# Optimization experiments

Measured on AMD Instinct MI355X. Metric: run time of the kernel, lower is better.

The kernel has to match this reference:

```python
import jax, jax.numpy as jnp
import numpy as np

N = 10000   # nodes (Hi-C bins)
E = 640000  # directed edges
H = 2       # attention heads
C = 512     # per-head out channels
NEG_SLOPE = 0.2

def _leaky_relu(v):
    return jnp.where(v >= 0, v, NEG_SLOPE * v)

def setup_inputs() -> dict:
    key = jax.random.key(0)
    ks = jax.random.split(key, 16)
    s = 0.02
    return {
        "x": jax.random.normal(ks[0], (N, 512), jnp.float32),
        "edge_index": jax.random.randint(ks[1], (2, E), 0, N, dtype=jnp.int64),
        "W": jax.random.normal(ks[2], (512, H * C), jnp.float32) * s,
        "att_src": jax.random.normal(ks[3], (H, C), jnp.float32) * s,
        "att_dst": jax.random.normal(ks[4], (H, C), jnp.float32) * s,
        "bias_conv": jnp.zeros((H * C,), jnp.float32),
        "Wa": jax.random.normal(ks[5], (1024, 256), jnp.float32) * s,
        "ba": jnp.zeros((256,), jnp.float32),
        "W1": jax.random.normal(ks[6], (256, 128), jnp.float32) * s,
        "b1": jnp.zeros((128,), jnp.float32),
        "W2": jax.random.normal(ks[7], (128, 64), jnp.float32) * s,
        "b2": jnp.zeros((64,), jnp.float32),
        "W3": jax.random.normal(ks[8], (64, 3), jnp.float32) * s,
        "b3": jnp.zeros((3,), jnp.float32),
    }

def reference(x, edge_index, W, att_src, att_dst, bias_conv,
              Wa, ba, W1, b1, W2, b2, W3, b3):
    n = x.shape[0]
    # PyG GATConv default: add self loops
    loop = jnp.arange(n, dtype=edge_index.dtype)
    src = jnp.concatenate([edge_index[0], loop])  # [E+N]
    dst = jnp.concatenate([edge_index[1], loop])
    # linear projection -> [N, H, C]
    h = (x @ W).reshape(n, H, C)
    a_src = jnp.einsum('nhc,hc->nh', h, att_src)  # [N, H]
    a_dst = jnp.einsum('nhc,hc->nh', h, att_dst)
    e = _leaky_relu(a_src[src] + a_dst[dst])      # [E+N, H]
    # segment softmax over destination nodes
    m = jax.ops.segment_max(e, dst, num_segments=n)
    ex = jnp.exp(e - m[dst])
    denom = jax.ops.segment_sum(ex, dst, num_segments=n)
    alpha = ex / denom[dst]                        # [E+N, H]
    # weighted scatter-add aggregation
    out = jax.ops.segment_sum(h[src] * alpha[..., None], dst, num_segments=n)
    out = out.reshape(n, H * C) + bias_conv        # concat heads -> [N, 1024]
    # MLP (dropout is identity in eval)
    y = jax.nn.relu(out)
    y = jax.nn.relu(y @ Wa + ba)
    y = jax.nn.relu(y @ W1 + b1)
    y = jax.nn.relu(y @ W2 + b2)
    y = y @ W3 + b3                                # [N, 3]
    # cdist p=2 via gram trick, grad-safe sqrt at 0
    sq = jnp.sum(y * y, axis=1)
    d2 = jnp.maximum(sq[:, None] + sq[None, :] - 2.0 * (y @ y.T), 0.0)
    pos = d2 > 0
    return jnp.where(pos, jnp.sqrt(jnp.where(pos, d2, 1.0)), 0.0)  # [N, N]
```

## Files before the change

kernel.cpp:

```cpp
#include <hip/hip_runtime.h>
#include <hip/hip_bf16.h>
#include <math.h>

#define N_NODES 10000
#define NE      640000
#define NTOT    (NE + N_NODES)
#define HC      1024
#define CC      512
#define SLOT    256

typedef __attribute__((ext_vector_type(8))) short bf16x8;
typedef __attribute__((ext_vector_type(4))) float f32x4;

__device__ __forceinline__ float lrelu(float v) { return v >= 0.f ? v : 0.2f * v; }

__device__ __forceinline__ void split1(float f, ushort& h, ushort& l) {
    unsigned u = __float_as_uint(f);
    unsigned hb = (u + 0x7FFFu + ((u >> 16) & 1u)) >> 16;
    float fh = __uint_as_float(hb << 16);
    float fl = f - fh;
    unsigned ul = __float_as_uint(fl);
    unsigned lb = (ul + 0x7FFFu + ((ul >> 16) & 1u)) >> 16;
    h = (ushort)hb; l = (ushort)lb;
}

__global__ __launch_bounds__(256) void transp_split(
    const float* __restrict__ Win, int K, int N,
    ushort* __restrict__ Th, ushort* __restrict__ Tl,
    float* __restrict__ zbuf, int zn)
{
    __shared__ float tile[32][33];
    int n0 = blockIdx.x * 32, k0 = blockIdx.y * 32;
    int tx = threadIdx.x & 31, ty = threadIdx.x >> 5;
    int gtid = (blockIdx.y * gridDim.x + blockIdx.x) * 256 + threadIdx.x;
    if (gtid < zn) zbuf[gtid] = 0.f;
    #pragma unroll
    for (int r = 0; r < 4; ++r)
        tile[ty + r * 8][tx] = Win[(size_t)(k0 + ty + r * 8) * N + n0 + tx];
    __syncthreads();
    #pragma unroll
    for (int r = 0; r < 4; ++r) {
        int n = ty + r * 8;
        float f = tile[tx][n];
        ushort h, l;
        split1(f, h, l);
        Th[(size_t)(n0 + n) * K + k0 + tx] = h;
        Tl[(size_t)(n0 + n) * K + k0 + tx] = l;
    }
}

template<int RELU_BIAS, int ATT, int SPLITA>
__global__ __launch_bounds__(256) void gemm_bf16x3(
    const ushort* __restrict__ Ah, const ushort* __restrict__ Al,
    const float* __restrict__ Af,
    const ushort* __restrict__ Bh, const ushort* __restrict__ Bl,
    const float* __restrict__ biasC,
    const float* __restrict__ attS, const float* __restrict__ attD,
    float* __restrict__ aS, float* __restrict__ aD,
    float* __restrict__ C, int M, int N, int K)
{
    __shared__ __align__(16) ushort sAh[4][128][8];
    __shared__ __align__(16) ushort sAl[4][128][8];
    __shared__ __align__(16) ushort sBh[4][128][8];
    __shared__ __align__(16) ushort sBl[4][128][8];
    const int bm = blockIdx.y * 128;
    const int bn = blockIdx.x * 128;
    const int tid = threadIdx.x;
    const int lane = tid & 63;
    const int w = tid >> 6;
    const int wm = (w >> 1) * 64, wn = (w & 1) * 64;
    const int l15 = lane & 15, l4 = lane >> 4;

    f32x4 acc[4][4];
    #pragma unroll
    for (int i = 0; i < 4; ++i)
        #pragma unroll
        for (int j = 0; j < 4; ++j)
            acc[i][j] = (f32x4){0.f, 0.f, 0.f, 0.f};

    for (int k0 = 0; k0 < K; k0 += 32) {
        #pragma unroll
        for (int qi = 0; qi < 4; ++qi) {
            int Q = qi * 256 + tid;
            int m = Q >> 3;
            int kq = (Q & 7) * 4;
            int gr = bm + m;
            ushort4 vh = make_ushort4(0, 0, 0, 0), vl = vh;
            if (SPLITA) {
                if (gr < M) {
                    float4 av = *(const float4*)(Af + (size_t)gr * K + k0 + kq);
                    split1(av.x, vh.x, vl.x);
                    split1(av.y, vh.y, vl.y);
                    split1(av.z, vh.z, vl.z);
                    split1(av.w, vh.w, vl.w);
                }
            } else if (gr < M) {
                vh = *(const ushort4*)(Ah + (size_t)gr * K + k0 + kq);
                vl = *(const ushort4*)(Al + (size_t)gr * K + k0 + kq);
            }
            *(ushort4*)&sAh[kq >> 3][m][kq & 7] = vh;
            *(ushort4*)&sAl[kq >> 3][m][kq & 7] = vl;
            ushort4 wh = *(const ushort4*)(Bh + (size_t)(bn + m) * K + k0 + kq);
            ushort4 wl = *(const ushort4*)(Bl + (size_t)(bn + m) * K + k0 + kq);
            *(ushort4*)&sBh[kq >> 3][m][kq & 7] = wh;
            *(ushort4*)&sBl[kq >> 3][m][kq & 7] = wl;
        }
        __syncthreads();
        bf16x8 ah[4], al[4], bh[4], bl[4];
        #pragma unroll
        for (int i = 0; i < 4; ++i) {
            ah[i] = *(const bf16x8*)&sAh[l4][wm + i * 16 + l15][0];
            al[i] = *(const bf16x8*)&sAl[l4][wm + i * 16 + l15][0];
            bh[i] = *(const bf16x8*)&sBh[l4][wn + i * 16 + l15][0];
            bl[i] = *(const bf16x8*)&sBl[l4][wn + i * 16 + l15][0];
        }
        #pragma unroll
        for (int i = 0; i < 4; ++i)
            #pragma unroll
            for (int j = 0; j < 4; ++j) {
                acc[i][j] = __builtin_amdgcn_mfma_f32_16x16x32_bf16(ah[i], bh[j], acc[i][j], 0, 0, 0);
                acc[i][j] = __builtin_amdgcn_mfma_f32_16x16x32_bf16(ah[i], bl[j], acc[i][j], 0, 0, 0);
                acc[i][j] = __builtin_amdgcn_mfma_f32_16x16x32_bf16(al[i], bh[j], acc[i][j], 0, 0, 0);
            }
        __syncthreads();
    }
    const int head = ATT ? ((bn + wn) >> 9) : 0;
    #pragma unroll
    for (int i = 0; i < 4; ++i) {
        #pragma unroll
        for (int r = 0; r < 4; ++r) {
            int row = bm + wm + i * 16 + l4 * 4 + r;
            if (row >= M) continue;
            float ps = 0.f, pd = 0.f;
            #pragma unroll
            for (int j = 0; j < 4; ++j) {
                int col = bn + wn + j * 16 + l15;
                float v = acc[i][j][r];
                if (RELU_BIAS) v = fmaxf(v + biasC[col], 0.f);
                C[(size_t)row * N + col] = v;
                if (ATT) {
                    int cc = col & (CC - 1);
                    ps += v * attS[head * CC + cc];
                    pd += v * attD[head * CC + cc];
                }
            }
            if (ATT) {
                #pragma unroll
                for (int o = 1; o < 16; o <<= 1) {
                    ps += __shfl_xor(ps, o);
                    pd += __shfl_xor(pd, o);
                }
                if (l15 == 0) {
                    atomicAdd(&aS[row * 2 + head], ps);
                    atomicAdd(&aD[row * 2 + head], pd);
                }
            }
        }
    }
}

template<int RELU_OUT, int MLP3>
__global__ __launch_bounds__(256) void gemm64(
    const float* __restrict__ A, const float* __restrict__ B,
    const float* __restrict__ biasC, float* __restrict__ C,
    const float* __restrict__ W3, const float* __restrict__ b3,
    float* __restrict__ y, float* __restrict__ sq,
    int M, int N, int K)
{
    __shared__ float As[16][68];
    __shared__ float Bs[16][68];
    const int bm = blockIdx.y * 64;
    const int bn = blockIdx.x * 64;
    const int tid = threadIdx.x;
    const int tx = tid & 15, ty = tid >> 4;

    const int arow  = tid >> 2;
    const int acol4 = (tid & 3) * 4;
    const int brow  = tid >> 4;
    const int bcol4 = (tid & 15) * 4;

    float acc[4][4] = {};

    for (int k0 = 0; k0 < K; k0 += 16) {
        int gr = bm + arow;
        float4 av = make_float4(0.f, 0.f, 0.f, 0.f);
        if (gr < M) av = *(const float4*)(A + (size_t)gr * K + k0 + acol4);
        As[acol4 + 0][arow] = av.x;
        As[acol4 + 1][arow] = av.y;
        As[acol4 + 2][arow] = av.z;
        As[acol4 + 3][arow] = av.w;
        float4 bv = *(const float4*)(B + (size_t)(k0 + brow) * N + bn + bcol4);
        *(float4*)&Bs[brow][bcol4] = bv;
        __syncthreads();
        #pragma unroll
        for (int k = 0; k < 16; ++k) {
            float a0 = As[k][ty * 4 + 0], a1 = As[k][ty * 4 + 1];
            float a2 = As[k][ty * 4 + 2], a3 = As[k][ty * 4 + 3];
            float b0 = Bs[k][tx * 4 + 0], b1 = Bs[k][tx * 4 + 1];
            float b2 = Bs[k][tx * 4 + 2], b3 = Bs[k][tx * 4 + 3];
            acc[0][0] += a0 * b0; acc[0][1] += a0 * b1; acc[0][2] += a0 * b2; acc[0][3] += a0 * b3;
            acc[1][0] += a1 * b0; acc[1][1] += a1 * b1; acc[1][2] += a1 * b2; acc[1][3] += a1 * b3;
            acc[2][0] += a2 * b0; acc[2][1] += a2 * b1; acc[2][2] += a2 * b2; acc[2][3] += a2 * b3;
            acc[3][0] += a3 * b0; acc[3][1] += a3 * b1; acc[3][2] += a3 * b2; acc[3][3] += a3 * b3;
        }
        __syncthreads();
    }
    #pragma unroll
    for (int i = 0; i < 4; ++i) {
        int row = bm + ty * 4 + i;
        if (row >= M) continue;
        if (MLP3) {
            float p0 = 0.f, p1 = 0.f, p2 = 0.f;
            #pragma unroll
            for (int j = 0; j < 4; ++j) {
                int col = tx * 4 + j;
                float v = fmaxf(acc[i][j] + biasC[col], 0.f);
                p0 += v * W3[col * 3 + 0];
                p1 += v * W3[col * 3 + 1];
                p2 += v * W3[col * 3 + 2];
            }
            #pragma unroll
            for (int o = 1; o < 16; o <<= 1) {
                p0 += __shfl_xor(p0, o);
                p1 += __shfl_xor(p1, o);
                p2 += __shfl_xor(p2, o);
            }
            if (tx == 0) {
                p0 += b3[0]; p1 += b3[1]; p2 += b3[2];
                y[row * 3 + 0] = p0; y[row * 3 + 1] = p1; y[row * 3 + 2] = p2;
                sq[row] = p0 * p0 + p1 * p1 + p2 * p2;
            }
        } else {
            #pragma unroll
            for (int j = 0; j < 4; ++j) {
                int col = bn + tx * 4 + j;
                float v = acc[i][j] + biasC[col];
                if (RELU_OUT) v = fmaxf(v, 0.f);
                C[(size_t)row * N + col] = v;
            }
        }
    }
}

__global__ __launch_bounds__(256) void scatter_stats(
    const int* __restrict__ ei,
    const float2* __restrict__ a_src2, const float2* __restrict__ a_dst2,
    int* __restrict__ cnt, float* __restrict__ denom,
    int2* __restrict__ pack0, int2* __restrict__ pack1)
{
    int e = blockIdx.x * blockDim.x + threadIdx.x;
    if (e >= NTOT) return;
    int s, d;
    if (e < NE) { s = ei[e]; d = ei[NE + e]; } else { s = d = e - NE; }
    float2 as = a_src2[s];
    float2 ad = a_dst2[d];
    float e0 = expf(lrelu(as.x + ad.x));
    float e1 = expf(lrelu(as.y + ad.y));
    int pos = atomicAdd(&cnt[d], 1);
    int slot = (d << 8) + pos;
    pack0[slot] = make_int2(s, __float_as_int(e0));
    pack1[slot] = make_int2(s, __float_as_int(e1));
    atomicAdd(&denom[d * 2 + 0], e0);
    atomicAdd(&denom[d * 2 + 1], e1);
}

__global__ __launch_bounds__(256) void aggregate_w4(
    const int* __restrict__ cnt,
    const int2* __restrict__ pack0, const int2* __restrict__ pack1,
    const float* __restrict__ denom, const float* __restrict__ bias_conv,
    const float* __restrict__ h,
    ushort* __restrict__ outh, ushort* __restrict__ outl)
{
    int wave = threadIdx.x >> 6;
    int lane = threadIdx.x & 63;
    int g    = lane >> 4;
    int l16  = lane & 15;
    int d = blockIdx.x * 4 + wave;
    int chunk = blockIdx.y;
    int cb = chunk * 64;
    int hd = chunk >> 3;
    const int2* __restrict__ pk = ((hd == 0) ? pack0 : pack1) + (d << 8);
    int cd = cnt[d];
    float inv = 1.f / denom[d * 2 + hd];
    const float* hbase = h + cb + l16 * 4;
    float4 ac0 = make_float4(0.f, 0.f, 0.f, 0.f);
    float4 ac1 = make_float4(0.f, 0.f, 0.f, 0.f);
    float4 ac2 = make_float4(0.f, 0.f, 0.f, 0.f);
    float4 ac3 = make_float4(0.f, 0.f, 0.f, 0.f);
    int i = g;
    for (; i + 12 < cd; i += 16) {
        int2 e0 = pk[i];
        int2 e1 = pk[i + 4];
        int2 e2 = pk[i + 8];
        int2 e3 = pk[i + 12];
        const float4 h0 = *(const float4*)(hbase + (size_t)e0.x * HC);
        const float4 h1 = *(const float4*)(hbase + (size_t)e1.x * HC);
        const float4 h2 = *(const float4*)(hbase + (size_t)e2.x * HC);
        const float4 h3 = *(const float4*)(hbase + (size_t)e3.x * HC);
        float a0 = __int_as_float(e0.y), a1 = __int_as_float(e1.y);
        float a2 = __int_as_float(e2.y), a3 = __int_as_float(e3.y);
        ac0.x += a0 * h0.x; ac0.y += a0 * h0.y; ac0.z += a0 * h0.z; ac0.w += a0 * h0.w;
        ac1.x += a1 * h1.x; ac1.y += a1 * h1.y; ac1.z += a1 * h1.z; ac1.w += a1 * h1.w;
        ac2.x += a2 * h2.x; ac2.y += a2 * h2.y; ac2.z += a2 * h2.z; ac2.w += a2 * h2.w;
        ac3.x += a3 * h3.x; ac3.y += a3 * h3.y; ac3.z += a3 * h3.z; ac3.w += a3 * h3.w;
    }
    for (; i < cd; i += 4) {
        int2 e0 = pk[i];
        float a0 = __int_as_float(e0.y);
        const float4 h0 = *(const float4*)(hbase + (size_t)e0.x * HC);
        ac0.x += a0 * h0.x; ac0.y += a0 * h0.y; ac0.z += a0 * h0.z; ac0.w += a0 * h0.w;
    }
    ac0.x += ac1.x + ac2.x + ac3.x;
    ac0.y += ac1.y + ac2.y + ac3.y;
    ac0.z += ac1.z + ac2.z + ac3.z;
    ac0.w += ac1.w + ac2.w + ac3.w;
    ac0.x += __shfl_xor(ac0.x, 16); ac0.y += __shfl_xor(ac0.y, 16);
    ac0.z += __shfl_xor(ac0.z, 16); ac0.w += __shfl_xor(ac0.w, 16);
    ac0.x += __shfl_xor(ac0.x, 32); ac0.y += __shfl_xor(ac0.y, 32);
    ac0.z += __shfl_xor(ac0.z, 32); ac0.w += __shfl_xor(ac0.w, 32);
    if (g == 0) {
        int c0 = cb + l16 * 4;
        float v[4];
        v[0] = fmaxf(ac0.x * inv + bias_conv[c0 + 0], 0.f);
        v[1] = fmaxf(ac0.y * inv + bias_conv[c0 + 1], 0.f);
        v[2] = fmaxf(ac0.z * inv + bias_conv[c0 + 2], 0.f);
        v[3] = fmaxf(ac0.w * inv + bias_conv[c0 + 3], 0.f);
        ushort hh[4], ll[4];
        #pragma unroll
        for (int j = 0; j < 4; ++j) split1(v[j], hh[j], ll[j]);
        *(ushort4*)(outh + (size_t)d * HC + c0) = make_ushort4(hh[0], hh[1], hh[2], hh[3]);
        *(ushort4*)(outl + (size_t)d * HC + c0) = make_ushort4(ll[0], ll[1], ll[2], ll[3]);
    }
}

__global__ __launch_bounds__(256) void pdist(
    const float* __restrict__ y, const float* __restrict__ sq,
    float* __restrict__ out)
{
    int i = blockIdx.y;
    int j0 = (blockIdx.x * 256 + threadIdx.x) * 4;
    if (j0 >= N_NODES) return;
    float yi0 = y[i * 3 + 0], yi1 = y[i * 3 + 1], yi2 = y[i * 3 + 2];
    float si = sq[i];
    float res[4];
    #pragma unroll
    for (int t = 0; t < 4; ++t) {
        int j = j0 + t;
        float d2 = si + sq[j] - 2.f * (yi0 * y[j * 3 + 0] + yi1 * y[j * 3 + 1] + yi2 * y[j * 3 + 2]);
        d2 = fmaxf(d2, 0.f);
        res[t] = d2 > 0.f ? sqrtf(d2) : 0.f;
    }
    *(float4*)(out + (size_t)i * N_NODES + j0) = make_float4(res[0], res[1], res[2], res[3]);
}

extern "C" void kernel_launch(void* const* d_in, const int* in_sizes, int n_in,
                              void* d_out, int out_size, void* d_ws, size_t ws_size,
                              hipStream_t stream) {
    const float* x         = (const float*)d_in[0];
    const int*   ei        = (const int*)d_in[1];
    const float* W         = (const float*)d_in[2];
    const float* att_src   = (const float*)d_in[3];
    const float* att_dst   = (const float*)d_in[4];
    const float* bias_conv = (const float*)d_in[5];
    const float* Wa        = (const float*)d_in[6];
    const float* ba        = (const float*)d_in[7];
    const float* W1        = (const float*)d_in[8];
    const float* b1        = (const float*)d_in[9];
    const float* W2        = (const float*)d_in[10];
    const float* b2        = (const float*)d_in[11];
    const float* W3        = (const float*)d_in[12];
    const float* b3        = (const float*)d_in[13];
    float* out = (float*)d_out;

    float*  h        = out;
    ushort* outh     = (ushort*)(out + 10240000);
    ushort* outl     = (ushort*)(out + 15360000);
    float*  y1       = out + 20480000;
    float*  y2       = out + 23040000;
    float*  a_src    = out + 24960000;
    float*  a_dst    = out + 24980000;
    int*    cnt      = (int*)(out + 25000000);
    float*  denom    = out + 25010240;
    int2*   pack0    = (int2*)(out + 25500000);
    int2*   pack1    = (int2*)(out + 30700000);
    ushort* Wth      = (ushort*)(out + 36000000);
    ushort* Wtl      = (ushort*)(out + 36300000);
    ushort* Wath     = (ushort*)(out + 36600000);
    ushort* Watl     = (ushort*)(out + 36800000);

    float* y  = (float*)d_ws;
    float* sq = (float*)d_ws + 30000;

    transp_split<<<dim3(1024 / 32, 512 / 32), 256, 0, stream>>>(
        W, 512, 1024, Wth, Wtl, a_src, 40000);
    transp_split<<<dim3(256 / 32, 1024 / 32), 256, 0, stream>>>(
        Wa, 1024, 256, Wath, Watl, (float*)cnt, 30240);

    gemm_bf16x3<0, 1, 1><<<dim3(1024 / 128, (N_NODES + 127) / 128), 256, 0, stream>>>(
        nullptr, nullptr, x, Wth, Wtl, nullptr, att_src, att_dst, a_src, a_dst,
        h, N_NODES, 1024, 512);

    scatter_stats<<<(NTOT + 255) / 256, 256, 0, stream>>>(
        ei, (const float2*)a_src, (const float2*)a_dst, cnt, denom, pack0, pack1);

    aggregate_w4<<<dim3(N_NODES / 4, 16), 256, 0, stream>>>(
        cnt, pack0, pack1, denom, bias_conv, h, outh, outl);

    gemm_bf16x3<1, 0, 0><<<dim3(256 / 128, (N_NODES + 127) / 128), 256, 0, stream>>>(
        outh, outl, nullptr, Wath, Watl, ba, nullptr, nullptr, nullptr, nullptr,
        y1, N_NODES, 256, 1024);
    gemm64<1, 0><<<dim3(128 / 64, (N_NODES + 63) / 64), 256, 0, stream>>>(
        y1, W1, b1, y2, nullptr, nullptr, nullptr, nullptr, N_NODES, 128, 256);
    gemm64<1, 1><<<dim3(1, (N_NODES + 63) / 64), 256, 0, stream>>>(
        y2, W2, b2, nullptr, W3, b3, y, sq, N_NODES, 64, 128);

    pdist<<<dim3((N_NODES + 1023) / 1024, N_NODES), 256, 0, stream>>>(y, sq, out);
}
```

Before: 551.8 us.

## Store h in per-chunk layout, fold softmax denom into aggregation, pack y with sq

The projection GEMM now writes h in a chunk-major layout ([16 chunks][N][64]), so each aggregation block gathers from a compact 2.5MB slice that fits in cache better. The softmax denominator is summed inside the aggregation loop instead of with float atomics in scatter_stats, which removes two atomics per edge and the denom buffer. y and its squared norm are packed into one float4 per node, so pdist does a single vector load per node instead of four scalar loads. The trade-off is that the alpha sum is recomputed by every chunk, 16 times per node.

```diff
diff --git a/kernel.cpp b/kernel.cpp
--- a/kernel.cpp
+++ b/kernel.cpp
@@ -8,6 +8,7 @@
 #define HC      1024
 #define CC      512
 #define SLOT    256
+#define CHN     (N_NODES * 64)
 
 typedef __attribute__((ext_vector_type(8))) short bf16x8;
 typedef __attribute__((ext_vector_type(4))) float f32x4;
@@ -137,11 +138,13 @@
                 int col = bn + wn + j * 16 + l15;
                 float v = acc[i][j][r];
                 if (RELU_BIAS) v = fmaxf(v + biasC[col], 0.f);
-                C[(size_t)row * N + col] = v;
                 if (ATT) {
+                    C[(size_t)(col >> 6) * CHN + (size_t)row * 64 + (col & 63)] = v;
                     int cc = col & (CC - 1);
                     ps += v * attS[head * CC + cc];
                     pd += v * attD[head * CC + cc];
+                } else {
+                    C[(size_t)row * N + col] = v;
                 }
             }
             if (ATT) {
@@ -164,7 +167,7 @@
     const float* __restrict__ A, const float* __restrict__ B,
     const float* __restrict__ biasC, float* __restrict__ C,
     const float* __restrict__ W3, const float* __restrict__ b3,
-    float* __restrict__ y, float* __restrict__ sq,
+    float4* __restrict__ y4,
     int M, int N, int K)
 {
     __shared__ float As[16][68];
@@ -227,8 +230,7 @@
             }
             if (tx == 0) {
                 p0 += b3[0]; p1 += b3[1]; p2 += b3[2];
-                y[row * 3 + 0] = p0; y[row * 3 + 1] = p1; y[row * 3 + 2] = p2;
-                sq[row] = p0 * p0 + p1 * p1 + p2 * p2;
+                y4[row] = make_float4(p0, p1, p2, p0 * p0 + p1 * p1 + p2 * p2);
             }
         } else {
             #pragma unroll
@@ -245,7 +247,7 @@
 __global__ __launch_bounds__(256) void scatter_stats(
     const int* __restrict__ ei,
     const float2* __restrict__ a_src2, const float2* __restrict__ a_dst2,
-    int* __restrict__ cnt, float* __restrict__ denom,
+    int* __restrict__ cnt,
     int2* __restrict__ pack0, int2* __restrict__ pack1)
 {
     int e = blockIdx.x * blockDim.x + threadIdx.x;
@@ -260,15 +262,13 @@
     int slot = (d << 8) + pos;
     pack0[slot] = make_int2(s, __float_as_int(e0));
     pack1[slot] = make_int2(s, __float_as_int(e1));
-    atomicAdd(&denom[d * 2 + 0], e0);
-    atomicAdd(&denom[d * 2 + 1], e1);
 }
 
 __global__ __launch_bounds__(256) void aggregate_w4(
     const int* __restrict__ cnt,
     const int2* __restrict__ pack0, const int2* __restrict__ pack1,
-    const float* __restrict__ denom, const float* __restrict__ bias_conv,
-    const float* __restrict__ h,
+    const float* __restrict__ bias_conv,
+    const float* __restrict__ hc,
     ushort* __restrict__ outh, ushort* __restrict__ outl)
 {
     int wave = threadIdx.x >> 6;
@@ -281,24 +281,25 @@
     int hd = chunk >> 3;
     const int2* __restrict__ pk = ((hd == 0) ? pack0 : pack1) + (d << 8);
     int cd = cnt[d];
-    float inv = 1.f / denom[d * 2 + hd];
-    const float* hbase = h + cb + l16 * 4;
+    const float* hbase = hc + (size_t)chunk * CHN + l16 * 4;
     float4 ac0 = make_float4(0.f, 0.f, 0.f, 0.f);
     float4 ac1 = make_float4(0.f, 0.f, 0.f, 0.f);
     float4 ac2 = make_float4(0.f, 0.f, 0.f, 0.f);
     float4 ac3 = make_float4(0.f, 0.f, 0.f, 0.f);
+    float asum = 0.f;
     int i = g;
     for (; i + 12 < cd; i += 16) {
         int2 e0 = pk[i];
         int2 e1 = pk[i + 4];
         int2 e2 = pk[i + 8];
         int2 e3 = pk[i + 12];
-        const float4 h0 = *(const float4*)(hbase + (size_t)e0.x * HC);
-        const float4 h1 = *(const float4*)(hbase + (size_t)e1.x * HC);
-        const float4 h2 = *(const float4*)(hbase + (size_t)e2.x * HC);
-        const float4 h3 = *(const float4*)(hbase + (size_t)e3.x * HC);
+        const float4 h0 = *(const float4*)(hbase + (size_t)e0.x * 64);
+        const float4 h1 = *(const float4*)(hbase + (size_t)e1.x * 64);
+        const float4 h2 = *(const float4*)(hbase + (size_t)e2.x * 64);
+        const float4 h3 = *(const float4*)(hbase + (size_t)e3.x * 64);
         float a0 = __int_as_float(e0.y), a1 = __int_as_float(e1.y);
         float a2 = __int_as_float(e2.y), a3 = __int_as_float(e3.y);
+        asum += a0 + a1 + a2 + a3;
         ac0.x += a0 * h0.x; ac0.y += a0 * h0.y; ac0.z += a0 * h0.z; ac0.w += a0 * h0.w;
         ac1.x += a1 * h1.x; ac1.y += a1 * h1.y; ac1.z += a1 * h1.z; ac1.w += a1 * h1.w;
         ac2.x += a2 * h2.x; ac2.y += a2 * h2.y; ac2.z += a2 * h2.z; ac2.w += a2 * h2.w;
@@ -307,7 +308,8 @@
     for (; i < cd; i += 4) {
         int2 e0 = pk[i];
         float a0 = __int_as_float(e0.y);
-        const float4 h0 = *(const float4*)(hbase + (size_t)e0.x * HC);
+        const float4 h0 = *(const float4*)(hbase + (size_t)e0.x * 64);
+        asum += a0;
         ac0.x += a0 * h0.x; ac0.y += a0 * h0.y; ac0.z += a0 * h0.z; ac0.w += a0 * h0.w;
     }
     ac0.x += ac1.x + ac2.x + ac3.x;
@@ -316,9 +318,12 @@
     ac0.w += ac1.w + ac2.w + ac3.w;
     ac0.x += __shfl_xor(ac0.x, 16); ac0.y += __shfl_xor(ac0.y, 16);
     ac0.z += __shfl_xor(ac0.z, 16); ac0.w += __shfl_xor(ac0.w, 16);
+    asum  += __shfl_xor(asum, 16);
     ac0.x += __shfl_xor(ac0.x, 32); ac0.y += __shfl_xor(ac0.y, 32);
     ac0.z += __shfl_xor(ac0.z, 32); ac0.w += __shfl_xor(ac0.w, 32);
+    asum  += __shfl_xor(asum, 32);
     if (g == 0) {
+        float inv = 1.f / asum;
         int c0 = cb + l16 * 4;
         float v[4];
         v[0] = fmaxf(ac0.x * inv + bias_conv[c0 + 0], 0.f);
@@ -334,19 +339,17 @@
 }
 
 __global__ __launch_bounds__(256) void pdist(
-    const float* __restrict__ y, const float* __restrict__ sq,
-    float* __restrict__ out)
+    const float4* __restrict__ y4, float* __restrict__ out)
 {
     int i = blockIdx.y;
     int j0 = (blockIdx.x * 256 + threadIdx.x) * 4;
     if (j0 >= N_NODES) return;
-    float yi0 = y[i * 3 + 0], yi1 = y[i * 3 + 1], yi2 = y[i * 3 + 2];
-    float si = sq[i];
+    float4 yi = y4[i];
     float res[4];
     #pragma unroll
     for (int t = 0; t < 4; ++t) {
-        int j = j0 + t;
-        float d2 = si + sq[j] - 2.f * (yi0 * y[j * 3 + 0] + yi1 * y[j * 3 + 1] + yi2 * y[j * 3 + 2]);
+        float4 yj = y4[j0 + t];
+        float d2 = yi.w + yj.w - 2.f * (yi.x * yj.x + yi.y * yj.y + yi.z * yj.z);
         d2 = fmaxf(d2, 0.f);
         res[t] = d2 > 0.f ? sqrtf(d2) : 0.f;
     }
@@ -372,7 +375,7 @@
     const float* b3        = (const float*)d_in[13];
     float* out = (float*)d_out;
 
-    float*  h        = out;
+    float*  hc       = out;
     ushort* outh     = (ushort*)(out + 10240000);
     ushort* outl     = (ushort*)(out + 15360000);
     float*  y1       = out + 20480000;
@@ -380,7 +383,6 @@
     float*  a_src    = out + 24960000;
     float*  a_dst    = out + 24980000;
     int*    cnt      = (int*)(out + 25000000);
-    float*  denom    = out + 25010240;
     int2*   pack0    = (int2*)(out + 25500000);
     int2*   pack1    = (int2*)(out + 30700000);
     ushort* Wth      = (ushort*)(out + 36000000);
@@ -388,31 +390,30 @@
     ushort* Wath     = (ushort*)(out + 36600000);
     ushort* Watl     = (ushort*)(out + 36800000);
 
-    float* y  = (float*)d_ws;
-    float* sq = (float*)d_ws + 30000;
+    float4* y4 = (float4*)d_ws;
 
     transp_split<<<dim3(1024 / 32, 512 / 32), 256, 0, stream>>>(
-        W, 512, 1024, Wth, Wtl, a_src, 40000);
+        W, 512, 1024, Wth, Wtl, a_src, 50240);
     transp_split<<<dim3(256 / 32, 1024 / 32), 256, 0, stream>>>(
-        Wa, 1024, 256, Wath, Watl, (float*)cnt, 30240);
+        Wa, 1024, 256, Wath, Watl, nullptr, 0);
 
     gemm_bf16x3<0, 1, 1><<<dim3(1024 / 128, (N_NODES + 127) / 128), 256, 0, stream>>>(
         nullptr, nullptr, x, Wth, Wtl, nullptr, att_src, att_dst, a_src, a_dst,
-        h, N_NODES, 1024, 512);
+        hc, N_NODES, 1024, 512);
 
     scatter_stats<<<(NTOT + 255) / 256, 256, 0, stream>>>(
-        ei, (const float2*)a_src, (const float2*)a_dst, cnt, denom, pack0, pack1);
+        ei, (const float2*)a_src, (const float2*)a_dst, cnt, pack0, pack1);
 
     aggregate_w4<<<dim3(N_NODES / 4, 16), 256, 0, stream>>>(
-        cnt, pack0, pack1, denom, bias_conv, h, outh, outl);
+        cnt, pack0, pack1, bias_conv, hc, outh, outl);
 
     gemm_bf16x3<1, 0, 0><<<dim3(256 / 128, (N_NODES + 127) / 128), 256, 0, stream>>>(
         outh, outl, nullptr, Wath, Watl, ba, nullptr, nullptr, nullptr, nullptr,
         y1, N_NODES, 256, 1024);
     gemm64<1, 0><<<dim3(128 / 64, (N_NODES + 63) / 64), 256, 0, stream>>>(
-        y1, W1, b1, y2, nullptr, nullptr, nullptr, nullptr, N_NODES, 128, 256);
+        y1, W1, b1, y2, nullptr, nullptr, nullptr, N_NODES, 128, 256);
     gemm64<1, 1><<<dim3(1, (N_NODES + 63) / 64), 256, 0, stream>>>(
-        y2, W2, b2, nullptr, W3, b3, y, sq, N_NODES, 64, 128);
-
-    pdist<<<dim3((N_NODES + 1023) / 1024, N_NODES), 256, 0, stream>>>(y, sq, out);
-}
+        y2, W2, b2, nullptr, W3, b3, y4, N_NODES, 64, 128);
+
+    pdist<<<dim3((N_NODES + 1023) / 1024, N_NODES), 256, 0, stream>>>(y4, out);
+}
```

After: 513.8 us. -6.9%, faster.
